# Optimization experiments

Hardware: AMD Instinct MI355X
Metric: run time of the kernel (lower is better)

Reference implementation:

```python
import jax, jax.numpy as jnp
import numpy as np

N = 50000      # nodes
E = 800000     # edges (before self loops)
IN = 128       # input_dim
H1, C1 = 4, 64   # conv1 heads, per-head channels (concat -> 256)
H2, C2 = 1, 64   # conv2 heads, per-head channels (concat=False -> 64)
EPS_BN = 1e-5
NEG_SLOPE = 0.2


def setup_inputs() -> dict:
    key = jax.random.key(0)
    ks = jax.random.split(key, 20)
    s = 0.05
    d = {}
    d["x"] = jax.random.normal(ks[0], (N, IN), dtype=jnp.float32)
    d["edge_index"] = jax.random.randint(ks[1], (2, E), 0, N, dtype=jnp.int32)
    # GATConv 1: lin weight [IN, H1*C1], att vectors [H1, C1], bias [H1*C1]
    d["W1"] = jax.random.normal(ks[2], (IN, H1 * C1), dtype=jnp.float32) * s
    d["a1_src"] = jax.random.normal(ks[3], (H1, C1), dtype=jnp.float32) * s
    d["a1_dst"] = jax.random.normal(ks[4], (H1, C1), dtype=jnp.float32) * s
    d["b1"] = jnp.zeros((H1 * C1,), jnp.float32)
    # GATConv 2 (concat=False): lin weight [H1*C1, H2*C2]
    d["W2"] = jax.random.normal(ks[5], (H1 * C1, H2 * C2), dtype=jnp.float32) * s
    d["a2_src"] = jax.random.normal(ks[6], (H2, C2), dtype=jnp.float32) * s
    d["a2_dst"] = jax.random.normal(ks[7], (H2, C2), dtype=jnp.float32) * s
    d["b2"] = jnp.zeros((C2,), jnp.float32)
    # projection Linear(output_dim -> input_dim)
    d["Wp"] = jax.random.normal(ks[8], (C2, IN), dtype=jnp.float32) * s
    d["bp"] = jnp.zeros((IN,), jnp.float32)
    # BatchNorm affine params
    d["g1"] = jnp.ones((H1 * C1,), jnp.float32); d["be1"] = jnp.zeros((H1 * C1,), jnp.float32)
    d["g2"] = jnp.ones((C2,), jnp.float32);      d["be2"] = jnp.zeros((C2,), jnp.float32)
    d["g3"] = jnp.ones((IN,), jnp.float32);      d["be3"] = jnp.zeros((IN,), jnp.float32)
    return d


def batch_norm(x, gamma, beta):
    mu = jnp.mean(x, axis=0, keepdims=True)
    var = jnp.var(x, axis=0, keepdims=True)
    return (x - mu) * jax.lax.rsqrt(var + EPS_BN) * gamma + beta


def gat_conv(x, src, dst, W, a_src, a_dst, bias, heads, out_ch, concat):
    n = x.shape[0]
    h = (x @ W).reshape(n, heads, out_ch)            # [N,H,C]
    alpha_s = jnp.einsum('nhc,hc->nh', h, a_src)     # [N,H]
    alpha_d = jnp.einsum('nhc,hc->nh', h, a_dst)
    e = jax.nn.leaky_relu(alpha_s[src] + alpha_d[dst], NEG_SLOPE)  # [E',H]
    # segment softmax over edges sharing the same destination node
    m = jax.ops.segment_max(e, dst, num_segments=n)
    m = jnp.where(jnp.isfinite(m), m, 0.0)
    ex = jnp.exp(e - m[dst])
    den = jax.ops.segment_sum(ex, dst, num_segments=n)
    alpha = ex / (den[dst] + 1e-16)                  # [E',H]
    msg = alpha[:, :, None] * h[src]                 # [E',H,C]
    out = jax.ops.segment_sum(msg, dst, num_segments=n)  # [N,H,C]
    if concat:
        out = out.reshape(n, heads * out_ch)
    else:
        out = out.mean(axis=1)
    return out + bias


def reference(x, edge_index, W1, a1_src, a1_dst, b1, W2, a2_src, a2_dst, b2,
              Wp, bp, g1, be1, g2, be2, g3, be3):
    n = x.shape[0]
    # PyG GATConv default add_self_loops=True
    loops = jnp.arange(n, dtype=edge_index.dtype)
    src = jnp.concatenate([edge_index[0], loops])
    dst = jnp.concatenate([edge_index[1], loops])
    h = gat_conv(x, src, dst, W1, a1_src, a1_dst, b1, H1, C1, True)
    h = jax.nn.elu(batch_norm(h, g1, be1))
    # dropout is a no-op in eval mode
    h = gat_conv(h, src, dst, W2, a2_src, a2_dst, b2, H2, C2, False)
    h = jax.nn.elu(batch_norm(h, g2, be2))
    h = h @ Wp + bp
    return batch_norm(h, g3, be3)
```

## Files before the change

kernel.cpp:

```cpp
#include <hip/hip_runtime.h>
#include <cstdint>
#include <cstddef>

#define NEG_SLOPE 0.2f
#define EPS_BN 1e-5f
#define CAP 128

typedef __bf16 bf16x8 __attribute__((ext_vector_type(8)));
typedef float  f32x4  __attribute__((ext_vector_type(4)));
typedef unsigned short ushort_t;

static __device__ __forceinline__ float lrelu(float x){ return x > 0.f ? x : NEG_SLOPE * x; }
static __device__ __forceinline__ float elu(float x){ return x > 0.f ? x : __expf(x) - 1.f; }

static __device__ __forceinline__ float bf2f(ushort_t u){
  union { unsigned i; float f; } c; c.i = ((unsigned)u) << 16; return c.f;
}
static __device__ __forceinline__ ushort_t f2bf(float f){
  unsigned u = __float_as_uint(f);
  u += 0x7fffu + ((u >> 16) & 1u);
  return (ushort_t)(u >> 16);
}
static __device__ __forceinline__ void unpk(unsigned u, float& lo, float& hi){
  lo = __uint_as_float(u << 16);
  hi = __uint_as_float(u & 0xffff0000u);
}

union BF8 { bf16x8 v; ushort_t u[8]; };

static inline int ceil_div(int a, int b){ return (a + b - 1) / b; }


__global__ void fill_u32_kernel(unsigned* __restrict__ p, unsigned v, int n){
  int i = blockIdx.x * 256 + threadIdx.x;
  if(i < n) p[i] = v;
}


__global__ void hist_kernel(const int* __restrict__ ei, int* __restrict__ deg, int E, int N){
  int e = blockIdx.x * 256 + threadIdx.x;
  if(e >= E + N) return;
  int d = (e < E) ? ei[E + e] : (e - E);
  atomicAdd(&deg[d], 1);
}

__global__ __launch_bounds__(256) void scan1_kernel(const int* __restrict__ deg, int* __restrict__ rowptr,
                                                    int* __restrict__ cur, int* __restrict__ partials, int n){
  int t = threadIdx.x, lane = t & 63, wv = t >> 6;
  int base = blockIdx.x * 2048 + t * 8;
  int v[8]; int run = 0;
  #pragma unroll
  for(int k = 0; k < 8; k++){ int i = base + k; v[k] = (i < n) ? deg[i] : 0; run += v[k]; }
  int sc = run;
  #pragma unroll
  for(int off = 1; off < 64; off <<= 1){
    int u = __shfl_up(sc, off);
    if(lane >= off) sc += u;
  }
  __shared__ int wtot[4], woff[4];
  if(lane == 63) wtot[wv] = sc;
  __syncthreads();
  if(t == 0){
    int a = 0;
    #pragma unroll
    for(int i = 0; i < 4; i++){ woff[i] = a; a += wtot[i]; }
    partials[blockIdx.x] = a;
  }
  __syncthreads();
  int excl = (sc - run) + woff[wv];
  #pragma unroll
  for(int k = 0; k < 8; k++){
    int i = base + k;
    if(i < n){ cur[i] = excl; excl += v[k]; rowptr[i + 1] = excl; }
  }
}

__global__ void scan2_kernel(int* __restrict__ partials, int nb){
  int lane = threadIdx.x;
  int v = (lane < nb) ? partials[lane] : 0;
  int sc = v;
  #pragma unroll
  for(int off = 1; off < 64; off <<= 1){
    int u = __shfl_up(sc, off);
    if(lane >= off) sc += u;
  }
  if(lane < nb) partials[lane] = sc - v;
}

__global__ void scan3_kernel(const int* __restrict__ partials, int* __restrict__ rowptr,
                             int* __restrict__ cur, int n){
  int i = blockIdx.x * 256 + threadIdx.x;
  if(i == 0) rowptr[0] = 0;
  if(i < n){
    int off = partials[i >> 11];
    rowptr[i + 1] += off;
    cur[i] += off;
  }
}

__global__ void scatter_kernel(const int* __restrict__ ei, int* __restrict__ cur,
                               int* __restrict__ col, int E, int N){
  int e = blockIdx.x * 256 + threadIdx.x;
  if(e >= E + N) return;
  int s, d;
  if(e < E){ s = ei[e]; d = ei[E + e]; } else { s = e - E; d = e - E; }
  int pos = atomicAdd(&cur[d], 1);
  col[pos] = s;
}


static __device__ void packW_body(const float* W, ushort_t* Wp, int K, int Nn, int idx){
  int lane = idx & 63;
  int rest = idx >> 6;
  int KS = K >> 5;
  int s = rest % KS, t = rest / KS;
  int n  = t * 16 + (lane & 15);
  int k0 = s * 32 + (lane >> 4) * 8;
  ushort_t tmp[8];
  #pragma unroll
  for(int j = 0; j < 8; j++) tmp[j] = f2bf(W[(size_t)(k0 + j) * Nn + n]);
  uint4 pk;
  pk.x = tmp[0] | ((unsigned)tmp[1] << 16);
  pk.y = tmp[2] | ((unsigned)tmp[3] << 16);
  pk.z = tmp[4] | ((unsigned)tmp[5] << 16);
  pk.w = tmp[6] | ((unsigned)tmp[7] << 16);
  *reinterpret_cast<uint4*>(Wp + (size_t)idx * 8) = pk;
}

__global__ void packW_all_kernel(const float* __restrict__ W1, const float* __restrict__ W2,
                                 const float* __restrict__ W3, ushort_t* __restrict__ W1p,
                                 ushort_t* __restrict__ W2p, ushort_t* __restrict__ W3p){
  int idx = blockIdx.x * 256 + threadIdx.x;
  if(idx < 4096)       packW_body(W1, W1p, 128, 256, idx);
  else if(idx < 6144)  packW_body(W2, W2p, 256, 64,  idx - 4096);
  else if(idx < 7168)  packW_body(W3, W3p, 64,  128, idx - 6144);
}


template<int K, int NT, int AMODE, int H>
__global__ __launch_bounds__(256) void gemm_kernel(const void* __restrict__ Asrc,
                                                   const ushort_t* __restrict__ Bp,
                                                   ushort_t* __restrict__ C, int M,
                                                   const float* __restrict__ scale,
                                                   const float* __restrict__ shift,
                                                   const float* __restrict__ a_src,
                                                   const float* __restrict__ a_dst,
                                                   float* __restrict__ as_,
                                                   float* __restrict__ ad_){
  constexpr int KS = K >> 5;
  int lane = threadIdx.x & 63, wv = threadIdx.x >> 6;
  int row0 = blockIdx.x * 64 + wv * 16;
  int mi = lane & 15, q = lane >> 4;
  int arow = row0 + mi; if(arow > M - 1) arow = M - 1;
  const bf16x8* bbase = reinterpret_cast<const bf16x8*>(Bp) + lane;
  f32x4 acc[NT] = {};
  #pragma unroll
  for(int s = 0; s < KS; s++){
    BF8 cv;
    if(AMODE == 0){
      const float* ap = (const float*)Asrc + (size_t)arow * K + s * 32 + q * 8;
      float4 u0 = *reinterpret_cast<const float4*>(ap);
      float4 u1 = *reinterpret_cast<const float4*>(ap + 4);
      cv.u[0] = f2bf(u0.x); cv.u[1] = f2bf(u0.y); cv.u[2] = f2bf(u0.z); cv.u[3] = f2bf(u0.w);
      cv.u[4] = f2bf(u1.x); cv.u[5] = f2bf(u1.y); cv.u[6] = f2bf(u1.z); cv.u[7] = f2bf(u1.w);
    } else {
      const ushort_t* ap = (const ushort_t*)Asrc + (size_t)arow * K + s * 32 + q * 8;
      uint4 u = *reinterpret_cast<const uint4*>(ap);
      int c0 = s * 32 + q * 8;
      float4 sc0 = *reinterpret_cast<const float4*>(scale + c0);
      float4 sc1 = *reinterpret_cast<const float4*>(scale + c0 + 4);
      float4 sh0 = *reinterpret_cast<const float4*>(shift + c0);
      float4 sh1 = *reinterpret_cast<const float4*>(shift + c0 + 4);
      float a, b;
      unpk(u.x, a, b); cv.u[0] = f2bf(elu(a * sc0.x + sh0.x)); cv.u[1] = f2bf(elu(b * sc0.y + sh0.y));
      unpk(u.y, a, b); cv.u[2] = f2bf(elu(a * sc0.z + sh0.z)); cv.u[3] = f2bf(elu(b * sc0.w + sh0.w));
      unpk(u.z, a, b); cv.u[4] = f2bf(elu(a * sc1.x + sh1.x)); cv.u[5] = f2bf(elu(b * sc1.y + sh1.y));
      unpk(u.w, a, b); cv.u[6] = f2bf(elu(a * sc1.z + sh1.z)); cv.u[7] = f2bf(elu(b * sc1.w + sh1.w));
    }
    bf16x8 af = cv.v;
    #pragma unroll
    for(int t = 0; t < NT; t++){
      bf16x8 bfr = bbase[((size_t)t * KS + s) * 64];
      acc[t] = __builtin_amdgcn_mfma_f32_16x16x32_bf16(af, bfr, acc[t], 0, 0, 0);
    }
  }
  #pragma unroll
  for(int t = 0; t < NT; t++){
    #pragma unroll
    for(int r = 0; r < 4; r++){
      int gr = row0 + q * 4 + r;
      if(gr < M) C[(size_t)gr * (NT * 16) + t * 16 + mi] = f2bf(acc[t][r]);
    }
  }
  if(H > 0){
    #pragma unroll
    for(int hh = 0; hh < H; hh++){
      #pragma unroll
      for(int r = 0; r < 4; r++){
        float ps = 0.f, pd = 0.f;
        #pragma unroll
        for(int tt = 0; tt < 4; tt++){
          int t = hh * 4 + tt;
          float av = acc[t][r];
          int c = t * 16 + mi;
          ps += av * a_src[c];
          pd += av * a_dst[c];
        }
        #pragma unroll
        for(int off = 1; off < 16; off <<= 1){
          ps += __shfl_xor(ps, off);
          pd += __shfl_xor(pd, off);
        }
        int gr = row0 + q * 4 + r;
        if(mi == 0 && gr < M){
          as_[(size_t)gr * H + hh] = ps;
          ad_[(size_t)gr * H + hh] = pd;
        }
      }
    }
  }
}


__global__ __launch_bounds__(256) void gat_agg4_kernel(const ushort_t* __restrict__ hfeat,
                                                       const float* __restrict__ as_,
                                                       const float* __restrict__ ad_,
                                                       const int* __restrict__ rowptr,
                                                       const int* __restrict__ col,
                                                       const float* __restrict__ bias,
                                                       ushort_t* __restrict__ out, int N){
  __shared__ float wsh[4][CAP * 4];
  int wid = threadIdx.x >> 6, lane = threadIdx.x & 63;
  int n = blockIdx.x * 4 + wid;
  if(n > N - 1) n = N - 1;
  int start = rowptr[n], end = rowptr[n + 1];
  float4 adn = *reinterpret_cast<const float4*>(ad_ + (size_t)n * 4);
  float d0 = 0.f, d1 = 0.f, d2 = 0.f, d3 = 0.f;
  for(int j = start + lane; j < end; j += 64){
    int s = col[j];
    float4 av = *reinterpret_cast<const float4*>(as_ + (size_t)s * 4);
    float w0 = __expf(lrelu(av.x + adn.x));
    float w1 = __expf(lrelu(av.y + adn.y));
    float w2 = __expf(lrelu(av.z + adn.z));
    float w3 = __expf(lrelu(av.w + adn.w));
    int jj = j - start;
    if(jj < CAP) *reinterpret_cast<float4*>(&wsh[wid][jj * 4]) = make_float4(w0, w1, w2, w3);
    d0 += w0; d1 += w1; d2 += w2; d3 += w3;
  }
  #pragma unroll
  for(int off = 32; off; off >>= 1){
    d0 += __shfl_xor(d0, off); d1 += __shfl_xor(d1, off);
    d2 += __shfl_xor(d2, off); d3 += __shfl_xor(d3, off);
  }
  __syncthreads();
  int g = lane >> 5, l = lane & 31, hidx = l >> 3;
  float den = (hidx == 0) ? d0 : (hidx == 1) ? d1 : (hidx == 2) ? d2 : d3;
  float dinv = 1.f / (den + 1e-16f);
  float adh = (hidx == 0) ? adn.x : (hidx == 1) ? adn.y : (hidx == 2) ? adn.z : adn.w;
  float acc[8] = {};
  auto body = [&](int j){
    int s = col[j];
    int jj = j - start;
    float wj = (jj < CAP) ? wsh[wid][jj * 4 + hidx]
                          : __expf(lrelu(as_[(size_t)s * 4 + hidx] + adh));
    uint4 u = *reinterpret_cast<const uint4*>(hfeat + (size_t)s * 256 + 8 * l);
    float a, b;
    unpk(u.x, a, b); acc[0] += wj * a; acc[1] += wj * b;
    unpk(u.y, a, b); acc[2] += wj * a; acc[3] += wj * b;
    unpk(u.z, a, b); acc[4] += wj * a; acc[5] += wj * b;
    unpk(u.w, a, b); acc[6] += wj * a; acc[7] += wj * b;
  };
  int j = start + g;
  for(; j + 2 < end; j += 4){ body(j); body(j + 2); }
  if(j < end) body(j);
  #pragma unroll
  for(int k = 0; k < 8; k++) acc[k] += __shfl_xor(acc[k], 32);
  int cbase = 8 * l + g * 4;
  ushort_t o0 = f2bf(acc[g * 4 + 0] * dinv + bias[cbase + 0]);
  ushort_t o1 = f2bf(acc[g * 4 + 1] * dinv + bias[cbase + 1]);
  ushort_t o2 = f2bf(acc[g * 4 + 2] * dinv + bias[cbase + 2]);
  ushort_t o3 = f2bf(acc[g * 4 + 3] * dinv + bias[cbase + 3]);
  uint2 pk; pk.x = o0 | ((unsigned)o1 << 16); pk.y = o2 | ((unsigned)o3 << 16);
  *reinterpret_cast<uint2*>(out + (size_t)n * 256 + cbase) = pk;
}


__global__ __launch_bounds__(256) void gat_agg1_kernel(const ushort_t* __restrict__ hfeat,
                                                       const float* __restrict__ as_,
                                                       const float* __restrict__ ad_,
                                                       const int* __restrict__ rowptr,
                                                       const int* __restrict__ col,
                                                       const float* __restrict__ bias,
                                                       ushort_t* __restrict__ out, int N){
  __shared__ float wsh[4][CAP];
  int wid = threadIdx.x >> 6, lane = threadIdx.x & 63;
  int n = blockIdx.x * 4 + wid;
  if(n > N - 1) n = N - 1;
  int start = rowptr[n], end = rowptr[n + 1];
  float adn = ad_[n];
  float den = 0.f;
  for(int j = start + lane; j < end; j += 64){
    int s = col[j];
    float w = __expf(lrelu(as_[s] + adn));
    int jj = j - start;
    if(jj < CAP) wsh[wid][jj] = w;
    den += w;
  }
  #pragma unroll
  for(int off = 32; off; off >>= 1) den += __shfl_xor(den, off);
  __syncthreads();
  float dinv = 1.f / (den + 1e-16f);
  int g = lane >> 4, l = lane & 15;
  float acc[4] = {};
  auto body = [&](int j){
    int s = col[j];
    int jj = j - start;
    float wj = (jj < CAP) ? wsh[wid][jj] : __expf(lrelu(as_[s] + adn));
    uint2 u = *reinterpret_cast<const uint2*>(hfeat + (size_t)s * 64 + 4 * l);
    float a, b;
    unpk(u.x, a, b); acc[0] += wj * a; acc[1] += wj * b;
    unpk(u.y, a, b); acc[2] += wj * a; acc[3] += wj * b;
  };
  int j = start + g;
  for(; j + 4 < end; j += 8){ body(j); body(j + 4); }
  if(j < end) body(j);
  #pragma unroll
  for(int k = 0; k < 4; k++){
    acc[k] += __shfl_xor(acc[k], 16);
    acc[k] += __shfl_xor(acc[k], 32);
  }
  if(g == 0){
    ushort_t o0 = f2bf(acc[0] * dinv + bias[4 * l + 0]);
    ushort_t o1 = f2bf(acc[1] * dinv + bias[4 * l + 1]);
    ushort_t o2 = f2bf(acc[2] * dinv + bias[4 * l + 2]);
    ushort_t o3 = f2bf(acc[3] * dinv + bias[4 * l + 3]);
    uint2 pk; pk.x = o0 | ((unsigned)o1 << 16); pk.y = o2 | ((unsigned)o3 << 16);
    *reinterpret_cast<uint2*>(out + (size_t)n * 64 + 4 * l) = pk;
  }
}


__global__ __launch_bounds__(256) void colstats_fin_kernel(const ushort_t* __restrict__ x, int N, int C,
                                                           float* __restrict__ stats,
                                                           const float* __restrict__ gamma,
                                                           const float* __restrict__ beta,
                                                           float* __restrict__ scale,
                                                           float* __restrict__ shift,
                                                           unsigned* __restrict__ ticket, int nblk){
  int t = threadIdx.x;
  int rpb = 256 / C;
  int c = t % C, rg = t / C;
  float sum = 0.f, sq = 0.f;
  for(int r = blockIdx.x * rpb + rg; r < N; r += gridDim.x * rpb){
    float v = bf2f(x[(size_t)r * C + c]);
    sum += v; sq += v * v;
  }
  __shared__ float ssum[256], ssq[256];
  ssum[t] = sum; ssq[t] = sq;
  __syncthreads();
  if(t < C){
    float S = 0.f, Q = 0.f;
    for(int g = 0; g < rpb; g++){ S += ssum[g * C + t]; Q += ssq[g * C + t]; }
    atomicAdd(&stats[t], S);
    atomicAdd(&stats[C + t], Q);
  }
  __shared__ bool is_last;
  __syncthreads();
  if(t == 0){
    __threadfence();
    unsigned prev = atomicAdd(ticket, 1u);
    is_last = (prev == (unsigned)(nblk - 1));
  }
  __syncthreads();
  if(is_last){
    for(int cc = t; cc < C; cc += 256){
      float S = atomicAdd(&stats[cc], 0.f);
      float Q = atomicAdd(&stats[C + cc], 0.f);
      float invN = 1.f / (float)N;
      float mu = S * invN;
      float var = Q * invN - mu * mu;
      float rs = rsqrtf(var + EPS_BN);
      float scl = rs * gamma[cc];
      scale[cc] = scl;
      shift[cc] = beta[cc] - mu * scl;
    }
  }
}


__global__ void bn3_kernel(const ushort_t* __restrict__ x, const float* __restrict__ scale,
                           const float* __restrict__ shift, float* __restrict__ y, long total, int cmask){
  long i = (long)blockIdx.x * 256 + threadIdx.x;
  if(i >= total) return;
  int c = (int)(i & (long)cmask);
  y[i] = bf2f(x[i]) * scale[c] + shift[c];
}


extern "C" void kernel_launch(void* const* d_in, const int* in_sizes, int n_in,
                              void* d_out, int out_size, void* d_ws, size_t ws_size,
                              hipStream_t stream){
  const float* x   = (const float*)d_in[0];
  const int*   ei  = (const int*)  d_in[1];
  const float* W1  = (const float*)d_in[2];
  const float* a1s = (const float*)d_in[3];
  const float* a1d = (const float*)d_in[4];
  const float* b1  = (const float*)d_in[5];
  const float* W2  = (const float*)d_in[6];
  const float* a2s = (const float*)d_in[7];
  const float* a2d = (const float*)d_in[8];
  const float* b2  = (const float*)d_in[9];
  const float* Wp  = (const float*)d_in[10];
  const float* g1  = (const float*)d_in[12]; const float* be1 = (const float*)d_in[13];
  const float* g2  = (const float*)d_in[14]; const float* be2 = (const float*)d_in[15];
  const float* g3  = (const float*)d_in[16]; const float* be3 = (const float*)d_in[17];
  float* out = (float*)d_out;

  const int N  = in_sizes[0] / 128;
  const int E  = in_sizes[1] / 2;
  const int EP = E + N;
  const int Mpad = ((N + 63) / 64) * 64;
  const int NB = ceil_div(N, 2048);

  char* p = (char*)d_ws;
  auto carve = [&](size_t bytes) -> char* {
    char* r = p; p += (bytes + 255) & ~(size_t)255; return r;
  };
  float* meta   = (float*)carve(2048 * 4);
  int*   deg    = (int*)carve((size_t)N * 4);
  int*   cur    = (int*)carve((size_t)N * 4);
  int*   rowptr = (int*)carve((size_t)(N + 1) * 4);
  int*   col    = (int*)carve((size_t)EP * 4);
  int*   part   = (int*)carve(64 * 4);
  float* as_    = (float*)carve((size_t)N * 4 * 4);
  float* ad_    = (float*)carve((size_t)N * 4 * 4);
  ushort_t* W1p = (ushort_t*)carve((size_t)128 * 256 * 2);
  ushort_t* W2p = (ushort_t*)carve((size_t)256 * 64 * 2);
  ushort_t* W3p = (ushort_t*)carve((size_t)64 * 128 * 2);
  ushort_t* h1b   = (ushort_t*)carve((size_t)Mpad * 256 * 2);
  ushort_t* out1b = (ushort_t*)carve((size_t)Mpad * 256 * 2);
  ushort_t* h2b   = (ushort_t*)carve((size_t)Mpad * 64 * 2);
  ushort_t* out2b = (ushort_t*)carve((size_t)Mpad * 64 * 2);
  ushort_t* h3b   = (ushort_t*)carve((size_t)Mpad * 128 * 2);

  float* stats1 = meta;        float* scale1 = meta + 512;  float* shift1 = meta + 768;
  float* stats2 = meta + 1024; float* scale2 = meta + 1152; float* shift2 = meta + 1216;
  float* stats3 = meta + 1280; float* scale3 = meta + 1536; float* shift3 = meta + 1664;
  unsigned* tick = (unsigned*)(meta + 1792);

  fill_u32_kernel<<<ceil_div(N + 2048, 256), 256, 0, stream>>>((unsigned*)meta, 0u, N + 2048);
  hist_kernel<<<ceil_div(EP, 256), 256, 0, stream>>>(ei, deg, E, N);
  scan1_kernel<<<NB, 256, 0, stream>>>(deg, rowptr, cur, part, N);
  scan2_kernel<<<1, 64, 0, stream>>>(part, NB);
  scan3_kernel<<<ceil_div(N, 256), 256, 0, stream>>>(part, rowptr, cur, N);
  scatter_kernel<<<ceil_div(EP, 256), 256, 0, stream>>>(ei, cur, col, E, N);
  packW_all_kernel<<<28, 256, 0, stream>>>(W1, W2, Wp, W1p, W2p, W3p);

  gemm_kernel<128, 16, 0, 4><<<Mpad / 64, 256, 0, stream>>>(x, W1p, h1b, N, nullptr, nullptr, a1s, a1d, as_, ad_);
  gat_agg4_kernel<<<ceil_div(N, 4), 256, 0, stream>>>(h1b, as_, ad_, rowptr, col, b1, out1b, N);
  colstats_fin_kernel<<<512, 256, 0, stream>>>(out1b, N, 256, stats1, g1, be1, scale1, shift1, tick + 0, 512);

  gemm_kernel<256, 4, 1, 1><<<Mpad / 64, 256, 0, stream>>>(out1b, W2p, h2b, N, scale1, shift1, a2s, a2d, as_, ad_);
  gat_agg1_kernel<<<ceil_div(N, 4), 256, 0, stream>>>(h2b, as_, ad_, rowptr, col, b2, out2b, N);
  colstats_fin_kernel<<<512, 256, 0, stream>>>(out2b, N, 64, stats2, g2, be2, scale2, shift2, tick + 1, 512);

  gemm_kernel<64, 8, 1, 0><<<Mpad / 64, 256, 0, stream>>>(out2b, W3p, h3b, N, scale2, shift2, nullptr, nullptr, nullptr, nullptr);
  colstats_fin_kernel<<<512, 256, 0, stream>>>(h3b, N, 128, stats3, g3, be3, scale3, shift3, tick + 2, 512);
  bn3_kernel<<<ceil_div(N * 128, 256), 256, 0, stream>>>(h3b, scale3, shift3, out, (long)N * 128, 127);
}
```

Measured before the change: 480.5 us.

## Fuse softmax denominator into aggregation, vectorize BN stats, merge scan passes

The GAT aggregation kernels drop the separate weight-precompute pass and shared-memory cache. They now compute each edge weight inline and accumulate the softmax denominator alongside the weighted feature sum, which saves one pass over the edge list per node and a block sync. The gat_agg4 loop is unrolled further. Column-stats and the final BN kernel use 8-wide and 4-wide vector loads, and scan2 is folded into scan1 through a last-block ticket, removing a launch. In exchange every lane recomputes its exp per head, and the tick+3 slot must already be zeroed by the initial fill.

```diff
diff --git a/kernel.cpp b/kernel.cpp
--- a/kernel.cpp
+++ b/kernel.cpp
@@ -4,7 +4,6 @@
 
 #define NEG_SLOPE 0.2f
 #define EPS_BN 1e-5f
-#define CAP 128
 
 typedef __bf16 bf16x8 __attribute__((ext_vector_type(8)));
 typedef float  f32x4  __attribute__((ext_vector_type(4)));
@@ -45,7 +44,8 @@
 }
 
 __global__ __launch_bounds__(256) void scan1_kernel(const int* __restrict__ deg, int* __restrict__ rowptr,
-                                                    int* __restrict__ cur, int* __restrict__ partials, int n){
+                                                    int* __restrict__ cur, int* __restrict__ partials,
+                                                    unsigned* __restrict__ tick, int n){
   int t = threadIdx.x, lane = t & 63, wv = t >> 6;
   int base = blockIdx.x * 2048 + t * 8;
   int v[8]; int run = 0;
@@ -58,6 +58,7 @@
     if(lane >= off) sc += u;
   }
   __shared__ int wtot[4], woff[4];
+  __shared__ bool slast;
   if(lane == 63) wtot[wv] = sc;
   __syncthreads();
   if(t == 0){
@@ -73,18 +74,22 @@
     int i = base + k;
     if(i < n){ cur[i] = excl; excl += v[k]; rowptr[i + 1] = excl; }
   }
-}
-
-__global__ void scan2_kernel(int* __restrict__ partials, int nb){
-  int lane = threadIdx.x;
-  int v = (lane < nb) ? partials[lane] : 0;
-  int sc = v;
-  #pragma unroll
-  for(int off = 1; off < 64; off <<= 1){
-    int u = __shfl_up(sc, off);
-    if(lane >= off) sc += u;
-  }
-  if(lane < nb) partials[lane] = sc - v;
+  if(t == 0){
+    __threadfence();
+    slast = (atomicAdd(tick, 1u) == (unsigned)(gridDim.x - 1));
+  }
+  __syncthreads();
+  if(slast && t < 64){
+    int nb = gridDim.x;
+    int pv = (t < nb) ? atomicAdd(&partials[t], 0) : 0;
+    int psc = pv;
+    #pragma unroll
+    for(int off = 1; off < 64; off <<= 1){
+      int u = __shfl_up(psc, off);
+      if(t >= off) psc += u;
+    }
+    if(t < nb) partials[t] = psc - pv;
+  }
 }
 
 __global__ void scan3_kernel(const int* __restrict__ partials, int* __restrict__ rowptr,
@@ -229,52 +234,32 @@
                                                        const int* __restrict__ col,
                                                        const float* __restrict__ bias,
                                                        ushort_t* __restrict__ out, int N){
-  __shared__ float wsh[4][CAP * 4];
   int wid = threadIdx.x >> 6, lane = threadIdx.x & 63;
   int n = blockIdx.x * 4 + wid;
   if(n > N - 1) n = N - 1;
   int start = rowptr[n], end = rowptr[n + 1];
-  float4 adn = *reinterpret_cast<const float4*>(ad_ + (size_t)n * 4);
-  float d0 = 0.f, d1 = 0.f, d2 = 0.f, d3 = 0.f;
-  for(int j = start + lane; j < end; j += 64){
-    int s = col[j];
-    float4 av = *reinterpret_cast<const float4*>(as_ + (size_t)s * 4);
-    float w0 = __expf(lrelu(av.x + adn.x));
-    float w1 = __expf(lrelu(av.y + adn.y));
-    float w2 = __expf(lrelu(av.z + adn.z));
-    float w3 = __expf(lrelu(av.w + adn.w));
-    int jj = j - start;
-    if(jj < CAP) *reinterpret_cast<float4*>(&wsh[wid][jj * 4]) = make_float4(w0, w1, w2, w3);
-    d0 += w0; d1 += w1; d2 += w2; d3 += w3;
-  }
-  #pragma unroll
-  for(int off = 32; off; off >>= 1){
-    d0 += __shfl_xor(d0, off); d1 += __shfl_xor(d1, off);
-    d2 += __shfl_xor(d2, off); d3 += __shfl_xor(d3, off);
-  }
-  __syncthreads();
   int g = lane >> 5, l = lane & 31, hidx = l >> 3;
-  float den = (hidx == 0) ? d0 : (hidx == 1) ? d1 : (hidx == 2) ? d2 : d3;
-  float dinv = 1.f / (den + 1e-16f);
-  float adh = (hidx == 0) ? adn.x : (hidx == 1) ? adn.y : (hidx == 2) ? adn.z : adn.w;
+  float adh = ad_[(size_t)n * 4 + hidx];
+  float den = 0.f;
   float acc[8] = {};
   auto body = [&](int j){
     int s = col[j];
-    int jj = j - start;
-    float wj = (jj < CAP) ? wsh[wid][jj * 4 + hidx]
-                          : __expf(lrelu(as_[(size_t)s * 4 + hidx] + adh));
+    float w = __expf(lrelu(as_[(size_t)s * 4 + hidx] + adh));
     uint4 u = *reinterpret_cast<const uint4*>(hfeat + (size_t)s * 256 + 8 * l);
+    den += w;
     float a, b;
-    unpk(u.x, a, b); acc[0] += wj * a; acc[1] += wj * b;
-    unpk(u.y, a, b); acc[2] += wj * a; acc[3] += wj * b;
-    unpk(u.z, a, b); acc[4] += wj * a; acc[5] += wj * b;
-    unpk(u.w, a, b); acc[6] += wj * a; acc[7] += wj * b;
+    unpk(u.x, a, b); acc[0] += w * a; acc[1] += w * b;
+    unpk(u.y, a, b); acc[2] += w * a; acc[3] += w * b;
+    unpk(u.z, a, b); acc[4] += w * a; acc[5] += w * b;
+    unpk(u.w, a, b); acc[6] += w * a; acc[7] += w * b;
   };
   int j = start + g;
-  for(; j + 2 < end; j += 4){ body(j); body(j + 2); }
-  if(j < end) body(j);
+  for(; j + 6 < end; j += 8){ body(j); body(j + 2); body(j + 4); body(j + 6); }
+  for(; j < end; j += 2) body(j);
+  den += __shfl_xor(den, 32);
   #pragma unroll
   for(int k = 0; k < 8; k++) acc[k] += __shfl_xor(acc[k], 32);
+  float dinv = 1.f / (den + 1e-16f);
   int cbase = 8 * l + g * 4;
   ushort_t o0 = f2bf(acc[g * 4 + 0] * dinv + bias[cbase + 0]);
   ushort_t o1 = f2bf(acc[g * 4 + 1] * dinv + bias[cbase + 1]);
@@ -292,43 +277,33 @@
                                                        const int* __restrict__ col,
                                                        const float* __restrict__ bias,
                                                        ushort_t* __restrict__ out, int N){
-  __shared__ float wsh[4][CAP];
   int wid = threadIdx.x >> 6, lane = threadIdx.x & 63;
   int n = blockIdx.x * 4 + wid;
   if(n > N - 1) n = N - 1;
   int start = rowptr[n], end = rowptr[n + 1];
+  int g = lane >> 4, l = lane & 15;
   float adn = ad_[n];
   float den = 0.f;
-  for(int j = start + lane; j < end; j += 64){
-    int s = col[j];
-    float w = __expf(lrelu(as_[s] + adn));
-    int jj = j - start;
-    if(jj < CAP) wsh[wid][jj] = w;
-    den += w;
-  }
-  #pragma unroll
-  for(int off = 32; off; off >>= 1) den += __shfl_xor(den, off);
-  __syncthreads();
-  float dinv = 1.f / (den + 1e-16f);
-  int g = lane >> 4, l = lane & 15;
   float acc[4] = {};
   auto body = [&](int j){
     int s = col[j];
-    int jj = j - start;
-    float wj = (jj < CAP) ? wsh[wid][jj] : __expf(lrelu(as_[s] + adn));
+    float w = __expf(lrelu(as_[s] + adn));
     uint2 u = *reinterpret_cast<const uint2*>(hfeat + (size_t)s * 64 + 4 * l);
+    den += w;
     float a, b;
-    unpk(u.x, a, b); acc[0] += wj * a; acc[1] += wj * b;
-    unpk(u.y, a, b); acc[2] += wj * a; acc[3] += wj * b;
+    unpk(u.x, a, b); acc[0] += w * a; acc[1] += w * b;
+    unpk(u.y, a, b); acc[2] += w * a; acc[3] += w * b;
   };
   int j = start + g;
   for(; j + 4 < end; j += 8){ body(j); body(j + 4); }
   if(j < end) body(j);
+  den += __shfl_xor(den, 16); den += __shfl_xor(den, 32);
   #pragma unroll
   for(int k = 0; k < 4; k++){
     acc[k] += __shfl_xor(acc[k], 16);
     acc[k] += __shfl_xor(acc[k], 32);
   }
+  float dinv = 1.f / (den + 1e-16f);
   if(g == 0){
     ushort_t o0 = f2bf(acc[0] * dinv + bias[4 * l + 0]);
     ushort_t o1 = f2bf(acc[1] * dinv + bias[4 * l + 1]);
@@ -340,27 +315,38 @@
 }
 
 
-__global__ __launch_bounds__(256) void colstats_fin_kernel(const ushort_t* __restrict__ x, int N, int C,
+template<int C>
+__global__ __launch_bounds__(256) void colstats_fin_kernel(const ushort_t* __restrict__ x, int N,
                                                            float* __restrict__ stats,
                                                            const float* __restrict__ gamma,
                                                            const float* __restrict__ beta,
                                                            float* __restrict__ scale,
                                                            float* __restrict__ shift,
                                                            unsigned* __restrict__ ticket, int nblk){
+  constexpr int TPR = C / 8;
+  constexpr int RPB = 256 / TPR;
   int t = threadIdx.x;
-  int rpb = 256 / C;
-  int c = t % C, rg = t / C;
-  float sum = 0.f, sq = 0.f;
-  for(int r = blockIdx.x * rpb + rg; r < N; r += gridDim.x * rpb){
-    float v = bf2f(x[(size_t)r * C + c]);
-    sum += v; sq += v * v;
-  }
-  __shared__ float ssum[256], ssq[256];
-  ssum[t] = sum; ssq[t] = sq;
+  int c0 = (t % TPR) * 8, rg = t / TPR;
+  float sum[8] = {}, sq[8] = {};
+  for(int r = blockIdx.x * RPB + rg; r < N; r += gridDim.x * RPB){
+    uint4 u = *reinterpret_cast<const uint4*>(x + (size_t)r * C + c0);
+    float a, b;
+    unpk(u.x, a, b); sum[0] += a; sq[0] += a * a; sum[1] += b; sq[1] += b * b;
+    unpk(u.y, a, b); sum[2] += a; sq[2] += a * a; sum[3] += b; sq[3] += b * b;
+    unpk(u.z, a, b); sum[4] += a; sq[4] += a * a; sum[5] += b; sq[5] += b * b;
+    unpk(u.w, a, b); sum[6] += a; sq[6] += a * a; sum[7] += b; sq[7] += b * b;
+  }
+  __shared__ float red[2][256][8];
+  #pragma unroll
+  for(int k = 0; k < 8; k++){ red[0][t][k] = sum[k]; red[1][t][k] = sq[k]; }
   __syncthreads();
   if(t < C){
+    int tr = t >> 3, k = t & 7;
     float S = 0.f, Q = 0.f;
-    for(int g = 0; g < rpb; g++){ S += ssum[g * C + t]; Q += ssq[g * C + t]; }
+    for(int g2 = 0; g2 < RPB; g2++){
+      S += red[0][g2 * TPR + tr][k];
+      Q += red[1][g2 * TPR + tr][k];
+    }
     atomicAdd(&stats[t], S);
     atomicAdd(&stats[C + t], Q);
   }
@@ -368,32 +354,37 @@
   __syncthreads();
   if(t == 0){
     __threadfence();
-    unsigned prev = atomicAdd(ticket, 1u);
-    is_last = (prev == (unsigned)(nblk - 1));
-  }
-  __syncthreads();
-  if(is_last){
-    for(int cc = t; cc < C; cc += 256){
-      float S = atomicAdd(&stats[cc], 0.f);
-      float Q = atomicAdd(&stats[C + cc], 0.f);
-      float invN = 1.f / (float)N;
-      float mu = S * invN;
-      float var = Q * invN - mu * mu;
-      float rs = rsqrtf(var + EPS_BN);
-      float scl = rs * gamma[cc];
-      scale[cc] = scl;
-      shift[cc] = beta[cc] - mu * scl;
-    }
+    is_last = (atomicAdd(ticket, 1u) == (unsigned)(nblk - 1));
+  }
+  __syncthreads();
+  if(is_last && t < C){
+    float S = atomicAdd(&stats[t], 0.f);
+    float Q = atomicAdd(&stats[C + t], 0.f);
+    float invN = 1.f / (float)N;
+    float mu = S * invN;
+    float var = Q * invN - mu * mu;
+    float rs = rsqrtf(var + EPS_BN);
+    float scl = rs * gamma[t];
+    scale[t] = scl;
+    shift[t] = beta[t] - mu * scl;
   }
 }
 
 
 __global__ void bn3_kernel(const ushort_t* __restrict__ x, const float* __restrict__ scale,
-                           const float* __restrict__ shift, float* __restrict__ y, long total, int cmask){
+                           const float* __restrict__ shift, float* __restrict__ y, long total4){
   long i = (long)blockIdx.x * 256 + threadIdx.x;
-  if(i >= total) return;
-  int c = (int)(i & (long)cmask);
-  y[i] = bf2f(x[i]) * scale[c] + shift[c];
+  if(i >= total4) return;
+  long e0 = i * 4;
+  int c0 = (int)(e0 & 127);
+  uint2 u = *reinterpret_cast<const uint2*>(x + e0);
+  float4 sc = *reinterpret_cast<const float4*>(scale + c0);
+  float4 sh = *reinterpret_cast<const float4*>(shift + c0);
+  float a, b;
+  float4 o;
+  unpk(u.x, a, b); o.x = a * sc.x + sh.x; o.y = b * sc.y + sh.y;
+  unpk(u.y, a, b); o.z = a * sc.z + sh.z; o.w = b * sc.w + sh.w;
+  *reinterpret_cast<float4*>(y + e0) = o;
 }
 
 
@@ -450,21 +441,20 @@
 
   fill_u32_kernel<<<ceil_div(N + 2048, 256), 256, 0, stream>>>((unsigned*)meta, 0u, N + 2048);
   hist_kernel<<<ceil_div(EP, 256), 256, 0, stream>>>(ei, deg, E, N);
-  scan1_kernel<<<NB, 256, 0, stream>>>(deg, rowptr, cur, part, N);
-  scan2_kernel<<<1, 64, 0, stream>>>(part, NB);
+  scan1_kernel<<<NB, 256, 0, stream>>>(deg, rowptr, cur, part, tick + 3, N);
   scan3_kernel<<<ceil_div(N, 256), 256, 0, stream>>>(part, rowptr, cur, N);
   scatter_kernel<<<ceil_div(EP, 256), 256, 0, stream>>>(ei, cur, col, E, N);
   packW_all_kernel<<<28, 256, 0, stream>>>(W1, W2, Wp, W1p, W2p, W3p);
 
   gemm_kernel<128, 16, 0, 4><<<Mpad / 64, 256, 0, stream>>>(x, W1p, h1b, N, nullptr, nullptr, a1s, a1d, as_, ad_);
   gat_agg4_kernel<<<ceil_div(N, 4), 256, 0, stream>>>(h1b, as_, ad_, rowptr, col, b1, out1b, N);
-  colstats_fin_kernel<<<512, 256, 0, stream>>>(out1b, N, 256, stats1, g1, be1, scale1, shift1, tick + 0, 512);
+  colstats_fin_kernel<256><<<512, 256, 0, stream>>>(out1b, N, stats1, g1, be1, scale1, shift1, tick + 0, 512);
 
   gemm_kernel<256, 4, 1, 1><<<Mpad / 64, 256, 0, stream>>>(out1b, W2p, h2b, N, scale1, shift1, a2s, a2d, as_, ad_);
   gat_agg1_kernel<<<ceil_div(N, 4), 256, 0, stream>>>(h2b, as_, ad_, rowptr, col, b2, out2b, N);
-  colstats_fin_kernel<<<512, 256, 0, stream>>>(out2b, N, 64, stats2, g2, be2, scale2, shift2, tick + 1, 512);
+  colstats_fin_kernel<64><<<512, 256, 0, stream>>>(out2b, N, stats2, g2, be2, scale2, shift2, tick + 1, 512);
 
   gemm_kernel<64, 8, 1, 0><<<Mpad / 64, 256, 0, stream>>>(out2b, W3p, h3b, N, scale2, shift2, nullptr, nullptr, nullptr, nullptr);
-  colstats_fin_kernel<<<512, 256, 0, stream>>>(h3b, N, 128, stats3, g3, be3, scale3, shift3, tick + 2, 512);
-  bn3_kernel<<<ceil_div(N * 128, 256), 256, 0, stream>>>(h3b, scale3, shift3, out, (long)N * 128, 127);
-}
+  colstats_fin_kernel<128><<<512, 256, 0, stream>>>(h3b, N, stats3, g3, be3, scale3, shift3, tick + 2, 512);
+  bn3_kernel<<<ceil_div(N * 128 / 4, 256), 256, 0, stream>>>(h3b, scale3, shift3, out, (long)N * 32);
+}
```

New measurement: 429.0 us. 1.12x faster.
